# Kernel tuning notes

Hardware: AMD Instinct MI355X
Metric: run time of the kernel (lower is better)

## Reference

```python
import jax, jax.numpy as jnp
import numpy as np
import math

B, S, D = 4, 4096, 1024
H = 16
HD = D // H          # head_dim = 64
M = 256              # nb_features (random projection dim)


def _orthogonal_gaussian(key, m, d):
    # FAVOR+ orthogonal random features: blocks of d orthogonal rows,
    # each row rescaled to a chi-distributed norm (norm of a d-dim gaussian).
    n_blocks = int(math.ceil(m / d))
    keys = jax.random.split(key, n_blocks + 1)
    blocks = []
    for i in range(n_blocks):
        g = jax.random.normal(keys[i], (d, d), dtype=jnp.float32)
        q, _ = jnp.linalg.qr(g)
        blocks.append(q.T)
    W = jnp.concatenate(blocks, axis=0)[:m]  # [m, d]
    norms = jnp.linalg.norm(
        jax.random.normal(keys[-1], (m, d), dtype=jnp.float32), axis=1, keepdims=True)
    return W * norms


def _softmax_kernel(x, proj, is_query, eps=1e-4):
    # x: [b,h,s,d]; proj: [m,d]. Standard FAVOR+ positive softmax features.
    d = x.shape[-1]
    ratio = proj.shape[0] ** -0.5
    x = x * (d ** -0.25)
    u = jnp.einsum('bhsd,md->bhsm', x, proj)  # projection
    diag = 0.5 * jnp.sum(x * x, axis=-1, keepdims=True)  # [b,h,s,1]
    if is_query:
        stab = jnp.max(u, axis=-1, keepdims=True)
    else:
        stab = jnp.max(u, axis=(-1, -2), keepdims=True)
    return ratio * (jnp.exp(u - diag - stab) + eps)


def performer_attention(Q, K, V, mask, proj):
    # Q,K,V: [b,h,s,d], mask: [b,s]
    scale = HD ** -0.25
    m4 = mask[:, None, :, None]
    Qs = Q * scale
    Ks = K * scale * m4
    Vs = V * m4
    q_prime = _softmax_kernel(Qs, proj, is_query=True)   # [b,h,s,m]
    k_prime = _softmax_kernel(Ks, proj, is_query=False)  # [b,h,s,m]
    # linear attention: O(s*m*d)
    kv = jnp.einsum('bhsm,bhsd->bhmd', k_prime, Vs)      # [b,h,m,d]
    z = 1.0 / (jnp.einsum('bhsm,bhm->bhs', q_prime, jnp.sum(k_prime, axis=2)) + 1e-6)
    out = jnp.einsum('bhsm,bhmd->bhsd', q_prime, kv) * z[..., None]
    return out


def setup_inputs() -> dict:
    key = jax.random.key(0)
    ks = jax.random.split(key, 9)
    X = jax.random.normal(ks[0], (B, S, D), dtype=jnp.float32)
    mask = jnp.ones((B, S), dtype=jnp.float32)
    s = D ** -0.5
    Wq = jax.random.normal(ks[1], (D, D), dtype=jnp.float32) * s
    bq = jnp.zeros((D,), dtype=jnp.float32)
    Wk = jax.random.normal(ks[2], (D, D), dtype=jnp.float32) * s
    bk = jnp.zeros((D,), dtype=jnp.float32)
    Wv = jax.random.normal(ks[3], (D, D), dtype=jnp.float32) * s
    bv = jnp.zeros((D,), dtype=jnp.float32)
    proj = _orthogonal_gaussian(ks[4], M, HD)
    return {"X": X, "mask": mask, "Wq": Wq, "bq": bq, "Wk": Wk, "bk": bk,
            "Wv": Wv, "bv": bv, "proj": proj}


def _split_heads(x):
    b, s, _ = x.shape
    return x.reshape(b, s, H, HD).transpose(0, 2, 1, 3)


def reference(X, mask, Wq, bq, Wk, bk, Wv, bv, proj):
    Q = _split_heads(X @ Wq + bq)
    K = _split_heads(X @ Wk + bk)
    V = _split_heads(X @ Wv + bv)
    attn = performer_attention(Q, K, V, mask, proj)  # [b,h,s,hd]
    out = attn.transpose(0, 2, 1, 3).reshape(B, S, D)
    return out
```

## Files before the change

kernel.cpp:

```cpp
#include <hip/hip_runtime.h>
#include <stdint.h>

#define DEVI static __device__ __forceinline__

typedef unsigned short u16;
typedef unsigned int u32;
typedef __attribute__((ext_vector_type(8))) short short8;
typedef __attribute__((ext_vector_type(4))) float f32x4;
typedef __attribute__((ext_vector_type(4))) unsigned short ushort4_t;

#define BB 4
#define SS 4096
#define DD 1024
#define HH 16
#define HDD 64
#define MM 256
#define BHN 64

DEVI u16 f2bf(float f) {
    u32 u = __float_as_uint(f);
    u += 0x7fffu + ((u >> 16) & 1u);
    return (u16)(u >> 16);
}
DEVI float bf2f(u16 h) { return __uint_as_float(((u32)h) << 16); }
DEVI u32 fenc(float f) {
    u32 u = __float_as_uint(f);
    return (u & 0x80000000u) ? ~u : (u | 0x80000000u);
}
DEVI float fdec(u32 k) {
    u32 u = (k & 0x80000000u) ? (k & 0x7fffffffu) : ~k;
    return __uint_as_float(u);
}

typedef __attribute__((address_space(1))) const unsigned int as1_u32;
typedef __attribute__((address_space(3))) unsigned int as3_u32;
DEVI void load_lds16(const void* g, void* lds) {
    __builtin_amdgcn_global_load_lds((as1_u32*)g, (as3_u32*)lds, 16, 0, 0);
}


__global__ void conv_bf16(const float* __restrict__ src, u16* __restrict__ dst, int n4) {
    int i = blockIdx.x * 256 + threadIdx.x;
    if (i < n4) {
        float4 v = reinterpret_cast<const float4*>(src)[i];
        ushort4_t o = { f2bf(v.x), f2bf(v.y), f2bf(v.z), f2bf(v.w) };
        reinterpret_cast<ushort4_t*>(dst)[i] = o;
    }
}

__global__ void conv_w(const float* __restrict__ Wq, const float* __restrict__ Wk,
                       const float* __restrict__ Wv, u16* __restrict__ Wt) {
    __shared__ float tile[64][65];
    const int jt = blockIdx.x, kt = blockIdx.y;
    const float* src = (jt < 16) ? Wq : (jt < 32) ? Wk : Wv;
    const int j0 = (jt & 15) * 64, k0 = kt * 64;
    const int t = threadIdx.x;
    for (int i = 0; i < 16; ++i) {
        int lin = t + i * 256;
        int kl = lin >> 6, jl = lin & 63;
        tile[kl][jl] = src[(size_t)(k0 + kl) * DD + j0 + jl];
    }
    __syncthreads();
    const int jg0 = jt * 64;
    for (int i = 0; i < 16; ++i) {
        int lin = t + i * 256;
        int jl = lin >> 6, kl = lin & 63;
        Wt[(size_t)(jg0 + jl) * DD + k0 + kl] = f2bf(tile[kl][jl]);
    }
}

__global__ __launch_bounds__(512, 2) void gemm1_big(
    const u16* __restrict__ Xbf, const u16* __restrict__ Wt,
    const float* __restrict__ bq, const float* __restrict__ bk, const float* __restrict__ bv,
    const float* __restrict__ mask,
    u16* __restrict__ Qh, u16* __restrict__ Kh, u16* __restrict__ Vt,
    float* __restrict__ dq, float* __restrict__ dk)
{
    extern __shared__ __align__(16) char smem[];
    const int tid = threadIdx.x, l = tid & 63, wv = tid >> 6;
    const int wm = wv >> 2, wn = wv & 3;
    const int bid = blockIdx.x;
    const int xcd = bid & 7, i6 = bid >> 3;
    const int bx = xcd * 8 + i6 / 12, by = i6 % 12;
    const int row0 = bx * 256, col0 = by * 256;

    const int srow = tid >> 3;
    const int scol = ((tid & 7) ^ (srow & 7)) * 8;

    #define ABUF(p) ((char*)smem + (p) * 32768)
    #define BBUF(p) ((char*)smem + 65536 + (p) * 32768)
    #define STA(p, kt, r) load_lds16(Xbf + (size_t)(row0 + (r)*64 + srow) * DD + (kt)*64 + scol, \
                                     ABUF(p) + (r)*8192 + wv*1024)
    #define STB(p, kt, r) load_lds16(Wt + (size_t)(col0 + (r)*64 + srow) * DD + (kt)*64 + scol, \
                                     BBUF(p) + (r)*8192 + wv*1024)

    STA(0,0,0); STA(0,0,1); STA(0,0,2); STA(0,0,3);
    STB(0,0,0); STB(0,0,1); STB(0,0,2); STB(0,0,3);
    asm volatile("s_waitcnt vmcnt(0)" ::: "memory");
    __builtin_amdgcn_s_barrier();
    __builtin_amdgcn_sched_barrier(0);

    f32x4 acc[8][4] = {};
    const int arow_b = wm * 128 + (l & 15);
    const int brow_b = wn * 64 + (l & 15);
    const int cb_b = (l >> 4) * 16;
    const int lx = (l & 7) << 4;

    for (int kt = 0; kt < 16; ++kt) {
        const int p = kt & 1, pn = p ^ 1;
        const bool more = (kt + 1) < 16;
        short8 bfr[4][2];
#pragma unroll
        for (int q = 0; q < 4; ++q) {
            if (more) {
                if (q == 0)      { STA(pn, kt + 1, 0); STA(pn, kt + 1, 1); }
                else if (q == 1) { STA(pn, kt + 1, 2); STA(pn, kt + 1, 3); }
                else if (q == 2) { STB(pn, kt + 1, 0); STB(pn, kt + 1, 1); }
                else             { STB(pn, kt + 1, 2); STB(pn, kt + 1, 3); }
            }
            if (q == 0) {
#pragma unroll
                for (int nf = 0; nf < 4; ++nf) {
                    const int br = brow_b + nf * 16;
#pragma unroll
                    for (int ks = 0; ks < 2; ++ks)
                        bfr[nf][ks] = *(const short8*)(BBUF(p) + br * 128 + ((cb_b + ks * 64) ^ lx));
                }
            }
            short8 a[2][2];
#pragma unroll
            for (int i = 0; i < 2; ++i) {
                const int ar = arow_b + (q * 2 + i) * 16;
#pragma unroll
                for (int ks = 0; ks < 2; ++ks)
                    a[i][ks] = *(const short8*)(ABUF(p) + ar * 128 + ((cb_b + ks * 64) ^ lx));
            }
            __builtin_amdgcn_s_setprio(1);
#pragma unroll
            for (int i = 0; i < 2; ++i)
#pragma unroll
                for (int nf = 0; nf < 4; ++nf) {
                    acc[q*2+i][nf] = __builtin_amdgcn_mfma_f32_16x16x32_bf16(a[i][0], bfr[nf][0], acc[q*2+i][nf], 0, 0, 0);
                    acc[q*2+i][nf] = __builtin_amdgcn_mfma_f32_16x16x32_bf16(a[i][1], bfr[nf][1], acc[q*2+i][nf], 0, 0, 0);
                }
            __builtin_amdgcn_s_setprio(0);
            __builtin_amdgcn_sched_barrier(0);
        }
        asm volatile("s_waitcnt vmcnt(0)" ::: "memory");
        __builtin_amdgcn_s_barrier();
        __builtin_amdgcn_sched_barrier(0);
    }

    const int region = by >> 2;
    const int h = ((by & 3) << 2) + wn;
    const int rg = row0 + wm * 128;
    const int b = rg >> 12;
    const int sb = rg & 4095;
    const size_t bh = (size_t)(b * HH + h);
    const int dd = l & 15;
    const int jbase = ((by & 3) << 8) + wn * 64;

    if (region == 0) {
        float bias[4];
#pragma unroll
        for (int nf = 0; nf < 4; ++nf) bias[nf] = bq[jbase + nf * 16 + dd];
#pragma unroll
        for (int mf = 0; mf < 8; ++mf) {
            float ds4[4];
#pragma unroll
            for (int g = 0; g < 4; ++g) {
                const int s = sb + mf * 16 + ((l >> 4) << 2) + g;
                float dsum = 0.f;
#pragma unroll
                for (int nf = 0; nf < 4; ++nf) {
                    u16 hv = f2bf((acc[mf][nf][g] + bias[nf]) * 0.125f);
                    Qh[(bh * SS + s) * HDD + nf * 16 + dd] = hv;
                    float fv = bf2f(hv);
                    dsum += fv * fv;
                }
                dsum += __shfl_xor(dsum, 1);
                dsum += __shfl_xor(dsum, 2);
                dsum += __shfl_xor(dsum, 4);
                dsum += __shfl_xor(dsum, 8);
                ds4[g] = 0.5f * dsum;
            }
            if (dd == 0)
                *(float4*)(dq + bh * SS + sb + mf * 16 + ((l >> 4) << 2)) =
                    make_float4(ds4[0], ds4[1], ds4[2], ds4[3]);
        }
    } else if (region == 1) {
        float bias[4];
#pragma unroll
        for (int nf = 0; nf < 4; ++nf) bias[nf] = bk[jbase + nf * 16 + dd];
#pragma unroll
        for (int mf = 0; mf < 8; ++mf) {
            float ds4[4];
#pragma unroll
            for (int g = 0; g < 4; ++g) {
                const int s = sb + mf * 16 + ((l >> 4) << 2) + g;
                const float m = mask[b * SS + s];
                float dsum = 0.f;
#pragma unroll
                for (int nf = 0; nf < 4; ++nf) {
                    u16 hv = f2bf((acc[mf][nf][g] + bias[nf]) * m * 0.125f);
                    Kh[(bh * SS + s) * HDD + nf * 16 + dd] = hv;
                    float fv = bf2f(hv);
                    dsum += fv * fv;
                }
                dsum += __shfl_xor(dsum, 1);
                dsum += __shfl_xor(dsum, 2);
                dsum += __shfl_xor(dsum, 4);
                dsum += __shfl_xor(dsum, 8);
                ds4[g] = 0.5f * dsum;
            }
            if (dd == 0)
                *(float4*)(dk + bh * SS + sb + mf * 16 + ((l >> 4) << 2)) =
                    make_float4(ds4[0], ds4[1], ds4[2], ds4[3]);
        }
    } else {
        float bias[4];
#pragma unroll
        for (int nf = 0; nf < 4; ++nf) bias[nf] = bv[jbase + nf * 16 + dd];
#pragma unroll
        for (int mf = 0; mf < 8; ++mf) {
            const int s0 = sb + mf * 16 + ((l >> 4) << 2);
#pragma unroll
            for (int nf = 0; nf < 4; ++nf) {
                ushort4_t pk;
#pragma unroll
                for (int g = 0; g < 4; ++g) {
                    const float m = mask[b * SS + s0 + g];
                    pk[g] = f2bf((acc[mf][nf][g] + bias[nf]) * m);
                }
                *(ushort4_t*)(Vt + (bh * HDD + nf * 16 + dd) * SS + s0) = pk;
            }
        }
    }
    #undef ABUF
    #undef BBUF
    #undef STA
    #undef STB
}

__global__ __launch_bounds__(256, 2) void stab_kernel(
    const u16* __restrict__ Kh, const u16* __restrict__ projb, u32* __restrict__ stabkey)
{
    __shared__ __align__(16) u16 Klds[64 * 64];
    __shared__ float red4[4];
    const int tid = threadIdx.x, l = tid & 63, wv = tid >> 6;
    const int rt = blockIdx.x, bh = blockIdx.y;
    short8 pb[4][2];
#pragma unroll
    for (int nf = 0; nf < 4; ++nf)
#pragma unroll
        for (int ks = 0; ks < 2; ++ks)
            pb[nf][ks] = *(const short8*)(projb + (wv * 64 + nf * 16 + (l & 15)) * HDD + ks * 32 + (l >> 4) * 8);
    const size_t sbase = (size_t)bh * SS + rt * 64;
#pragma unroll
    for (int c = 0; c < 2; ++c) {
        const int rb = wv * 16 + c * 8;
        const int r = rb + (l >> 3);
        load_lds16(Kh + (sbase + r) * HDD + (((l & 7) ^ (r & 7)) * 8), (char*)Klds + rb * 128);
    }
    __syncthreads();
    float mx = -3.0e38f;
#pragma unroll
    for (int sf = 0; sf < 4; ++sf) {
        const int s = sf * 16 + (l & 15);
        f32x4 u4[4] = {};
#pragma unroll
        for (int ks = 0; ks < 2; ++ks) {
            short8 ak = *(const short8*)((const char*)Klds + s * 128 + ((ks * 64 + (l >> 4) * 16) ^ ((s & 7) << 4)));
#pragma unroll
            for (int nf = 0; nf < 4; ++nf)
                u4[nf] = __builtin_amdgcn_mfma_f32_16x16x32_bf16(ak, pb[nf][ks], u4[nf], 0, 0, 0);
        }
#pragma unroll
        for (int nf = 0; nf < 4; ++nf)
#pragma unroll
            for (int g = 0; g < 4; ++g) mx = fmaxf(mx, u4[nf][g]);
    }
#pragma unroll
    for (int o = 1; o < 64; o <<= 1) mx = fmaxf(mx, __shfl_xor(mx, o));
    if (l == 0) red4[wv] = mx;
    __syncthreads();
    if (tid == 0) {
        float m2 = fmaxf(fmaxf(red4[0], red4[1]), fmaxf(red4[2], red4[3]));
        atomicMax(stabkey + bh, fenc(m2));
    }
}

__global__ __launch_bounds__(256, 2) void kv_fused(
    const u16* __restrict__ Kh, const u16* __restrict__ Vt,
    const u16* __restrict__ projb, const float* __restrict__ dk,
    const u32* __restrict__ stabkey,
    float* __restrict__ kv_part, float* __restrict__ ksum_part)
{
    __shared__ __align__(16) u16 Klds[64 * 64];
    __shared__ __align__(16) u16 Vlds[64 * 64];
    __shared__ __align__(16) u16 Kp[256 * 64];
    const int tid = threadIdx.x, l = tid & 63, wv = tid >> 6;
    const int ck = blockIdx.x, bh = blockIdx.y;
    const float stab = fdec(stabkey[bh]);
    short8 pb[4][2];
#pragma unroll
    for (int nf = 0; nf < 4; ++nf)
#pragma unroll
        for (int ks = 0; ks < 2; ++ks)
            pb[nf][ks] = *(const short8*)(projb + (wv * 64 + nf * 16 + (l & 15)) * HDD + ks * 32 + (l >> 4) * 8);
    f32x4 acc[4][4] = {};
    float ksc[4] = {0.f, 0.f, 0.f, 0.f};
    const size_t sbase = (size_t)bh * SS + ck * 512;
    for (int it = 0; it < 8; ++it) {
        const int s0 = it * 64;
#pragma unroll
        for (int c = 0; c < 2; ++c) {
            const int rb = wv * 16 + c * 8;
            const int r = rb + (l >> 3);
            const int sc = ((l & 7) ^ (r & 7)) * 8;
            load_lds16(Kh + (sbase + s0 + r) * HDD + sc, (char*)Klds + rb * 128);
            load_lds16(Vt + ((size_t)bh * HDD + r) * SS + ck * 512 + s0 + sc, (char*)Vlds + rb * 128);
        }
        __syncthreads();
#pragma unroll
        for (int sf = 0; sf < 4; ++sf) {
            const int s = sf * 16 + (l & 15);
            f32x4 u4[4] = {};
#pragma unroll
            for (int ks = 0; ks < 2; ++ks) {
                short8 ak = *(const short8*)((const char*)Klds + s * 128 + ((ks * 64 + (l >> 4) * 16) ^ ((s & 7) << 4)));
#pragma unroll
                for (int nf = 0; nf < 4; ++nf)
                    u4[nf] = __builtin_amdgcn_mfma_f32_16x16x32_bf16(ak, pb[nf][ks], u4[nf], 0, 0, 0);
            }
            const int srow = sf * 16 + (l >> 4) * 4;
            const float4 dkv = *(const float4*)(dk + sbase + s0 + srow);
#pragma unroll
            for (int nf = 0; nf < 4; ++nf) {
                const int m = wv * 64 + nf * 16 + (l & 15);
                u16 h0 = f2bf(0.0625f * (__expf(u4[nf][0] - dkv.x - stab) + 1e-4f));
                u16 h1 = f2bf(0.0625f * (__expf(u4[nf][1] - dkv.y - stab) + 1e-4f));
                u16 h2 = f2bf(0.0625f * (__expf(u4[nf][2] - dkv.z - stab) + 1e-4f));
                u16 h3 = f2bf(0.0625f * (__expf(u4[nf][3] - dkv.w - stab) + 1e-4f));
                ksc[nf] += bf2f(h0) + bf2f(h1) + bf2f(h2) + bf2f(h3);
                uint2 w; w.x = (u32)h0 | ((u32)h1 << 16); w.y = (u32)h2 | ((u32)h3 << 16);
                *(uint2*)((char*)Kp + m * 128 + ((srow * 2) ^ ((m & 7) << 4))) = w;
            }
        }
#pragma unroll
        for (int ks = 0; ks < 2; ++ks) {
            short8 am[4], bv8[4];
#pragma unroll
            for (int mf = 0; mf < 4; ++mf) {
                const int m = wv * 64 + mf * 16 + (l & 15);
                am[mf] = *(const short8*)((const char*)Kp + m * 128 + ((ks * 64 + (l >> 4) * 16) ^ ((m & 7) << 4)));
            }
#pragma unroll
            for (int nf = 0; nf < 4; ++nf) {
                const int d = nf * 16 + (l & 15);
                bv8[nf] = *(const short8*)((const char*)Vlds + d * 128 + ((ks * 64 + (l >> 4) * 16) ^ ((d & 7) << 4)));
            }
#pragma unroll
            for (int mf = 0; mf < 4; ++mf)
#pragma unroll
                for (int nf = 0; nf < 4; ++nf)
                    acc[mf][nf] = __builtin_amdgcn_mfma_f32_16x16x32_bf16(am[mf], bv8[nf], acc[mf][nf], 0, 0, 0);
        }
        __syncthreads();
    }
    const size_t pbase = (size_t)ck * BHN + bh;
#pragma unroll
    for (int nf = 0; nf < 4; ++nf) {
        float v = ksc[nf];
        v += __shfl_xor(v, 16);
        v += __shfl_xor(v, 32);
        if (l < 16) ksum_part[pbase * MM + wv * 64 + nf * 16 + l] = v;
    }
#pragma unroll
    for (int mf = 0; mf < 4; ++mf)
#pragma unroll
        for (int nf = 0; nf < 4; ++nf)
            *(f32x4*)(kv_part + (pbase * HDD + nf * 16 + (l & 15)) * MM + wv * 64 + mf * 16 + (l >> 4) * 4) = acc[mf][nf];
}

__global__ void reduceB2(const float* __restrict__ kv_part, const float* __restrict__ ksum_part,
                         u16* __restrict__ Bmat) {
    const int bh = blockIdx.x, n = blockIdx.y, t = threadIdx.x;
    float s = 0.f;
    if (n < 64) {
#pragma unroll
        for (int ck = 0; ck < 8; ++ck) s += kv_part[(((size_t)ck * BHN + bh) * HDD + n) * MM + t];
    } else if (n == 64) {
#pragma unroll
        for (int ck = 0; ck < 8; ++ck) s += ksum_part[((size_t)ck * BHN + bh) * MM + t];
    }
    Bmat[((size_t)bh * 80 + n) * MM + t] = (n <= 64) ? f2bf(s) : (u16)0;
}

__global__ __launch_bounds__(256, 2) void out_fused(
    const u16* __restrict__ Qh, const u16* __restrict__ projb,
    const float* __restrict__ dq, const u16* __restrict__ Bmat,
    float* __restrict__ out)
{
    __shared__ __align__(16) u16 Blds[80 * 256];
    __shared__ __align__(16) u16 Qlds[32 * 64];
    __shared__ __align__(16) u16 qlds[32 * 256];
    __shared__ float red[4][32];
    const int tid = threadIdx.x, l = tid & 63, wv = tid >> 6;
    const int rt = blockIdx.x, bh = blockIdx.y;
#pragma unroll
    for (int c = 0; c < 10; ++c) {
        const int r = (wv * 10 + c) * 2 + (l >> 5);
        load_lds16(Bmat + (size_t)bh * 20480 + r * 256 + (((l & 31) ^ (r & 7)) * 8),
                   (char*)Blds + (wv * 10 + c) * 1024);
    }
    const size_t srowbase = (size_t)bh * SS + rt * 32;
    {
        const int rb = wv * 8;
        const int r = rb + (l >> 3);
        load_lds16(Qh + (srowbase + r) * HDD + (((l & 7) ^ (r & 7)) * 8), (char*)Qlds + rb * 128);
    }
    short8 pa[4][2];
#pragma unroll
    for (int mf = 0; mf < 4; ++mf)
#pragma unroll
        for (int ks = 0; ks < 2; ++ks)
            pa[mf][ks] = *(const short8*)(projb + (wv * 64 + mf * 16 + (l & 15)) * HDD + ks * 32 + (l >> 4) * 8);
    __syncthreads();
    f32x4 u[4][2] = {};
#pragma unroll
    for (int ks = 0; ks < 2; ++ks) {
        short8 bq8[2];
#pragma unroll
        for (int nf = 0; nf < 2; ++nf) {
            const int s = nf * 16 + (l & 15);
            bq8[nf] = *(const short8*)((const char*)Qlds + s * 128 + ((ks * 64 + (l >> 4) * 16) ^ ((s & 7) << 4)));
        }
#pragma unroll
        for (int mf = 0; mf < 4; ++mf)
#pragma unroll
            for (int nf = 0; nf < 2; ++nf)
                u[mf][nf] = __builtin_amdgcn_mfma_f32_16x16x32_bf16(pa[mf][ks], bq8[nf], u[mf][nf], 0, 0, 0);
    }
#pragma unroll
    for (int nf = 0; nf < 2; ++nf) {
        float v = -3.0e38f;
#pragma unroll
        for (int mf = 0; mf < 4; ++mf)
#pragma unroll
            for (int g = 0; g < 4; ++g) v = fmaxf(v, u[mf][nf][g]);
        v = fmaxf(v, __shfl_xor(v, 16));
        v = fmaxf(v, __shfl_xor(v, 32));
        if ((l >> 4) == 0) red[wv][nf * 16 + l] = v;
    }
    __syncthreads();
#pragma unroll
    for (int nf = 0; nf < 2; ++nf) {
        const int s = nf * 16 + (l & 15);
        const float mx = fmaxf(fmaxf(red[0][s], red[1][s]), fmaxf(red[2][s], red[3][s]));
        const float dg = dq[srowbase + s];
#pragma unroll
        for (int mf = 0; mf < 4; ++mf) {
            u16 h0 = f2bf(0.0625f * (__expf(u[mf][nf][0] - dg - mx) + 1e-4f));
            u16 h1 = f2bf(0.0625f * (__expf(u[mf][nf][1] - dg - mx) + 1e-4f));
            u16 h2 = f2bf(0.0625f * (__expf(u[mf][nf][2] - dg - mx) + 1e-4f));
            u16 h3 = f2bf(0.0625f * (__expf(u[mf][nf][3] - dg - mx) + 1e-4f));
            uint2 w; w.x = (u32)h0 | ((u32)h1 << 16); w.y = (u32)h2 | ((u32)h3 << 16);
            const int mb = (wv * 64 + mf * 16 + (l >> 4) * 4) * 2;
            *(uint2*)((char*)qlds + s * 512 + (mb ^ ((s & 7) << 4))) = w;
        }
    }
    __syncthreads();
    f32x4 acc[2][2] = {};
    for (int kt = 0; kt < 8; ++kt) {
        short8 aq[2], bb[2];
#pragma unroll
        for (int mf = 0; mf < 2; ++mf) {
            const int s = mf * 16 + (l & 15);
            aq[mf] = *(const short8*)((const char*)qlds + s * 512 + ((kt * 64 + (l >> 4) * 16) ^ ((s & 7) << 4)));
        }
        {
            const int n0 = wv * 16 + (l & 15);
            bb[0] = *(const short8*)((const char*)Blds + n0 * 512 + ((kt * 64 + (l >> 4) * 16) ^ ((n0 & 7) << 4)));
            const int n1 = 64 + (l & 15);
            bb[1] = *(const short8*)((const char*)Blds + n1 * 512 + ((kt * 64 + (l >> 4) * 16) ^ ((n1 & 7) << 4)));
        }
#pragma unroll
        for (int mf = 0; mf < 2; ++mf)
#pragma unroll
            for (int nf = 0; nf < 2; ++nf)
                acc[mf][nf] = __builtin_amdgcn_mfma_f32_16x16x32_bf16(aq[mf], bb[nf], acc[mf][nf], 0, 0, 0);
    }
    const int b = bh >> 4, h = bh & 15;
#pragma unroll
    for (int mf = 0; mf < 2; ++mf) {
#pragma unroll
        for (int g = 0; g < 4; ++g) {
            const float den = __shfl(acc[mf][1][g], (l & 48));
            const float z = 1.0f / (den + 1e-6f);
            const int s = rt * 32 + mf * 16 + (l >> 4) * 4 + g;
            out[((size_t)b * SS + s) * DD + h * HDD + wv * 16 + (l & 15)] = acc[mf][0][g] * z;
        }
    }
}

extern "C" void kernel_launch(void* const* d_in, const int* in_sizes, int n_in,
                              void* d_out, int out_size, void* d_ws, size_t ws_size,
                              hipStream_t stream)
{
    const float* X    = (const float*)d_in[0];
    const float* mask = (const float*)d_in[1];
    const float* Wq   = (const float*)d_in[2];
    const float* bq   = (const float*)d_in[3];
    const float* Wk   = (const float*)d_in[4];
    const float* bk   = (const float*)d_in[5];
    const float* Wv   = (const float*)d_in[6];
    const float* bv   = (const float*)d_in[7];
    const float* proj = (const float*)d_in[8];
    float* out = (float*)d_out;

    char* p = (char*)d_ws;
    u16* Xbf = (u16*)p;
    float* kv_part = (float*)p; p += 33554432;
    u16* Wt = (u16*)p;    p += 6291456;
    u16* projb = (u16*)p; p += 32768;
    u16* Qh = (u16*)p;    p += 33554432;
    u16* Kh = (u16*)p;    p += 33554432;
    u16* Vt = (u16*)p;    p += 33554432;
    float* dq = (float*)p; p += 1048576;
    float* dk = (float*)p; p += 1048576;
    u32* stabkey = (u32*)p; p += 256;
    float* ksum_part = (float*)p; p += 524288;
    u16* Bmat = (u16*)p;  p += 2621440;
    if (ws_size < 145785088ull) return;

    hipFuncSetAttribute((const void*)gemm1_big, hipFuncAttributeMaxDynamicSharedMemorySize, 131072);

    hipMemsetAsync(stabkey, 0, 256, stream);
    conv_bf16<<<16384, 256, 0, stream>>>(X, Xbf, 4194304);
    conv_w<<<dim3(48, 16), 256, 0, stream>>>(Wq, Wk, Wv, Wt);
    conv_bf16<<<16, 256, 0, stream>>>(proj, projb, 4096);
    gemm1_big<<<768, 512, 131072, stream>>>(Xbf, Wt, bq, bk, bv, mask, Qh, Kh, Vt, dq, dk);
    stab_kernel<<<dim3(64, 64), 256, 0, stream>>>(Kh, projb, stabkey);
    kv_fused<<<dim3(8, 64), 256, 0, stream>>>(Kh, Vt, projb, dk, stabkey, kv_part, ksum_part);
    reduceB2<<<dim3(64, 80), 256, 0, stream>>>(kv_part, ksum_part, Bmat);
    out_fused<<<dim3(128, 64), 256, 0, stream>>>(Qh, projb, dq, Bmat, out);
}
```

Before: 298.4 us.

## Use K=32 tiles with 4-stage LDS pipeline in QKV projection GEMM

The QKV projection GEMM's K step shrinks from 64 to 32. The LDS ring grows from double to quadruple buffering, so loads are issued three iterations ahead and waits use partial vmcnt counts instead of draining to zero. The LDS layout is remapped so that two 32-wide rows pack into each 128-byte line with an XOR swizzle, giving one short8 read per fragment. The aim is to hide global load latency better, at the cost of twice as many barriers and a more intricate address mapping.

Measured after the change: 305.1 us. 2.2% more time.

```diff
diff --git a/kernel.cpp b/kernel.cpp
--- a/kernel.cpp
+++ b/kernel.cpp
@@ -69,7 +69,7 @@
     }
 }
 
-__global__ __launch_bounds__(512, 2) void gemm1_big(
+__global__ __launch_bounds__(512, 2) void gemm1_k32(
     const u16* __restrict__ Xbf, const u16* __restrict__ Wt,
     const float* __restrict__ bq, const float* __restrict__ bk, const float* __restrict__ bv,
     const float* __restrict__ mask,
@@ -84,71 +84,72 @@
     const int bx = xcd * 8 + i6 / 12, by = i6 % 12;
     const int row0 = bx * 256, col0 = by * 256;
 
-    const int srow = tid >> 3;
-    const int scol = ((tid & 7) ^ (srow & 7)) * 8;
-
-    #define ABUF(p) ((char*)smem + (p) * 32768)
-    #define BBUF(p) ((char*)smem + 65536 + (p) * 32768)
-    #define STA(p, kt, r) load_lds16(Xbf + (size_t)(row0 + (r)*64 + srow) * DD + (kt)*64 + scol, \
-                                     ABUF(p) + (r)*8192 + wv*1024)
-    #define STB(p, kt, r) load_lds16(Wt + (size_t)(col0 + (r)*64 + srow) * DD + (kt)*64 + scol, \
-                                     BBUF(p) + (r)*8192 + wv*1024)
-
-    STA(0,0,0); STA(0,0,1); STA(0,0,2); STA(0,0,3);
-    STB(0,0,0); STB(0,0,1); STB(0,0,2); STB(0,0,3);
-    asm volatile("s_waitcnt vmcnt(0)" ::: "memory");
+    int sA[2];
+#pragma unroll
+    for (int j = 0; j < 2; ++j) {
+        const int o = j * 8192 + tid * 16;
+        const int R = o >> 7;
+        const int logpos = (o & 127) ^ ((R & 7) << 4);
+        const int r = 2 * R + (logpos >> 6);
+        const int c8 = (logpos >> 4) & 3;
+        sA[j] = r * DD + c8 * 8;
+    }
+    const size_t xbase = (size_t)row0 * DD;
+    const size_t wbase = (size_t)col0 * DD;
+
+    #define ABUF(b) ((char*)smem + (b) * 16384)
+    #define BBUF(b) ((char*)smem + 65536 + (b) * 16384)
+    #define STA(b, kt, j) load_lds16(Xbf + xbase + (kt) * 32 + sA[j], ABUF(b) + (j) * 8192 + wv * 1024)
+    #define STB(b, kt, j) load_lds16(Wt + wbase + (kt) * 32 + sA[j], BBUF(b) + (j) * 8192 + wv * 1024)
+
+#pragma unroll
+    for (int t = 0; t < 3; ++t) { STA(t, t, 0); STA(t, t, 1); STB(t, t, 0); STB(t, t, 1); }
+    asm volatile("s_waitcnt vmcnt(8)" ::: "memory");
     __builtin_amdgcn_s_barrier();
     __builtin_amdgcn_sched_barrier(0);
 
     f32x4 acc[8][4] = {};
-    const int arow_b = wm * 128 + (l & 15);
-    const int brow_b = wn * 64 + (l & 15);
-    const int cb_b = (l >> 4) * 16;
-    const int lx = (l & 7) << 4;
-
-    for (int kt = 0; kt < 16; ++kt) {
-        const int p = kt & 1, pn = p ^ 1;
-        const bool more = (kt + 1) < 16;
-        short8 bfr[4][2];
+    const int hl = (l & 15) >> 1;
+    const int xorc = hl << 4;
+    const int pa = ((wm * 64 + hl) * 128 + (l & 1) * 64 + (l >> 4) * 16) ^ xorc;
+    const int pb = ((wn * 32 + hl) * 128 + (l & 1) * 64 + (l >> 4) * 16) ^ xorc;
+
+    for (int kt = 0; kt < 32; ++kt) {
+        const int p = kt & 3, pn = (kt + 3) & 3;
+        const bool more = (kt + 3) < 32;
+        short8 bfr[4];
 #pragma unroll
         for (int q = 0; q < 4; ++q) {
             if (more) {
-                if (q == 0)      { STA(pn, kt + 1, 0); STA(pn, kt + 1, 1); }
-                else if (q == 1) { STA(pn, kt + 1, 2); STA(pn, kt + 1, 3); }
-                else if (q == 2) { STB(pn, kt + 1, 0); STB(pn, kt + 1, 1); }
-                else             { STB(pn, kt + 1, 2); STB(pn, kt + 1, 3); }
+                if (q == 0)      STA(pn, kt + 3, 0);
+                else if (q == 1) STA(pn, kt + 3, 1);
+                else if (q == 2) STB(pn, kt + 3, 0);
+                else             STB(pn, kt + 3, 1);
             }
             if (q == 0) {
 #pragma unroll
-                for (int nf = 0; nf < 4; ++nf) {
-                    const int br = brow_b + nf * 16;
-#pragma unroll
-                    for (int ks = 0; ks < 2; ++ks)
-                        bfr[nf][ks] = *(const short8*)(BBUF(p) + br * 128 + ((cb_b + ks * 64) ^ lx));
-                }
-            }
-            short8 a[2][2];
-#pragma unroll
-            for (int i = 0; i < 2; ++i) {
-                const int ar = arow_b + (q * 2 + i) * 16;
-#pragma unroll
-                for (int ks = 0; ks < 2; ++ks)
-                    a[i][ks] = *(const short8*)(ABUF(p) + ar * 128 + ((cb_b + ks * 64) ^ lx));
-            }
+                for (int nf = 0; nf < 4; ++nf)
+                    bfr[nf] = *(const short8*)(BBUF(p) + pb + nf * 1024);
+            }
+            short8 a[2];
+#pragma unroll
+            for (int i = 0; i < 2; ++i)
+                a[i] = *(const short8*)(ABUF(p) + pa + (q * 2 + i) * 1024);
             __builtin_amdgcn_s_setprio(1);
 #pragma unroll
             for (int i = 0; i < 2; ++i)
 #pragma unroll
-                for (int nf = 0; nf < 4; ++nf) {
-                    acc[q*2+i][nf] = __builtin_amdgcn_mfma_f32_16x16x32_bf16(a[i][0], bfr[nf][0], acc[q*2+i][nf], 0, 0, 0);
-                    acc[q*2+i][nf] = __builtin_amdgcn_mfma_f32_16x16x32_bf16(a[i][1], bfr[nf][1], acc[q*2+i][nf], 0, 0, 0);
-                }
+                for (int nf = 0; nf < 4; ++nf)
+                    acc[q * 2 + i][nf] = __builtin_amdgcn_mfma_f32_16x16x32_bf16(a[i], bfr[nf], acc[q * 2 + i][nf], 0, 0, 0);
             __builtin_amdgcn_s_setprio(0);
+        }
+        if (kt < 31) {
+            if (kt + 3 < 32)      asm volatile("s_waitcnt vmcnt(8)" ::: "memory");
+            else if (kt + 2 < 32) asm volatile("s_waitcnt vmcnt(4)" ::: "memory");
+            else                  asm volatile("s_waitcnt vmcnt(0)" ::: "memory");
+            __builtin_amdgcn_s_barrier();
             __builtin_amdgcn_sched_barrier(0);
         }
-        asm volatile("s_waitcnt vmcnt(0)" ::: "memory");
-        __builtin_amdgcn_s_barrier();
-        __builtin_amdgcn_sched_barrier(0);
     }
 
     const int region = by >> 2;
@@ -534,13 +535,13 @@
     u16* Bmat = (u16*)p;  p += 2621440;
     if (ws_size < 145785088ull) return;
 
-    hipFuncSetAttribute((const void*)gemm1_big, hipFuncAttributeMaxDynamicSharedMemorySize, 131072);
+    hipFuncSetAttribute((const void*)gemm1_k32, hipFuncAttributeMaxDynamicSharedMemorySize, 131072);
 
     hipMemsetAsync(stabkey, 0, 256, stream);
     conv_bf16<<<16384, 256, 0, stream>>>(X, Xbf, 4194304);
     conv_w<<<dim3(48, 16), 256, 0, stream>>>(Wq, Wk, Wv, Wt);
     conv_bf16<<<16, 256, 0, stream>>>(proj, projb, 4096);
-    gemm1_big<<<768, 512, 131072, stream>>>(Xbf, Wt, bq, bk, bv, mask, Qh, Kh, Vt, dq, dk);
+    gemm1_k32<<<768, 512, 131072, stream>>>(Xbf, Wt, bq, bk, bv, mask, Qh, Kh, Vt, dq, dk);
     stab_kernel<<<dim3(64, 64), 256, 0, stream>>>(Kh, projb, stabkey);
     kv_fused<<<dim3(8, 64), 256, 0, stream>>>(Kh, Vt, projb, dk, stabkey, kv_part, ksum_part);
     reduceB2<<<dim3(64, 80), 256, 0, stream>>>(kv_part, ksum_part, Bmat);
```

## Fold key stabilizer into kv pass with per-chunk local max and rescale in reduce

Applied to the files above, without the earlier changes.

Drops the separate stab_kernel, its atomicMax and the memset. Each kv_fused block now computes a per-wave local max over its 512-row chunk, using triple-buffered async K loads, and then builds kv and ksum against that local stabilizer. The epsilon term is moved out via a separately accumulated V sum. reduceB3 rescales each chunk's partials by exp(local-global) and adds the eps and ratio terms. out_fused now processes 64 rows per block and reads Bmat straight from global memory instead of staging it in LDS. The cost is a second pass over K per chunk inside kv_fused and a change in numerics from per-chunk stabilization.

New measurement: 260.1 us. -12.8%, faster.

```diff
diff --git a/kernel.cpp b/kernel.cpp
--- a/kernel.cpp
+++ b/kernel.cpp
@@ -23,14 +23,6 @@
     return (u16)(u >> 16);
 }
 DEVI float bf2f(u16 h) { return __uint_as_float(((u32)h) << 16); }
-DEVI u32 fenc(float f) {
-    u32 u = __float_as_uint(f);
-    return (u & 0x80000000u) ? ~u : (u | 0x80000000u);
-}
-DEVI float fdec(u32 k) {
-    u32 u = (k & 0x80000000u) ? (k & 0x7fffffffu) : ~k;
-    return __uint_as_float(u);
-}
 
 typedef __attribute__((address_space(1))) const unsigned int as1_u32;
 typedef __attribute__((address_space(3))) unsigned int as3_u32;
@@ -242,111 +234,121 @@
     #undef STB
 }
 
-__global__ __launch_bounds__(256, 2) void stab_kernel(
-    const u16* __restrict__ Kh, const u16* __restrict__ projb, u32* __restrict__ stabkey)
-{
-    __shared__ __align__(16) u16 Klds[64 * 64];
-    __shared__ float red4[4];
-    const int tid = threadIdx.x, l = tid & 63, wv = tid >> 6;
-    const int rt = blockIdx.x, bh = blockIdx.y;
-    short8 pb[4][2];
-#pragma unroll
-    for (int nf = 0; nf < 4; ++nf)
-#pragma unroll
-        for (int ks = 0; ks < 2; ++ks)
-            pb[nf][ks] = *(const short8*)(projb + (wv * 64 + nf * 16 + (l & 15)) * HDD + ks * 32 + (l >> 4) * 8);
-    const size_t sbase = (size_t)bh * SS + rt * 64;
-#pragma unroll
-    for (int c = 0; c < 2; ++c) {
-        const int rb = wv * 16 + c * 8;
-        const int r = rb + (l >> 3);
-        load_lds16(Kh + (sbase + r) * HDD + (((l & 7) ^ (r & 7)) * 8), (char*)Klds + rb * 128);
-    }
-    __syncthreads();
-    float mx = -3.0e38f;
-#pragma unroll
-    for (int sf = 0; sf < 4; ++sf) {
-        const int s = sf * 16 + (l & 15);
-        f32x4 u4[4] = {};
-#pragma unroll
-        for (int ks = 0; ks < 2; ++ks) {
-            short8 ak = *(const short8*)((const char*)Klds + s * 128 + ((ks * 64 + (l >> 4) * 16) ^ ((s & 7) << 4)));
-#pragma unroll
-            for (int nf = 0; nf < 4; ++nf)
-                u4[nf] = __builtin_amdgcn_mfma_f32_16x16x32_bf16(ak, pb[nf][ks], u4[nf], 0, 0, 0);
-        }
-#pragma unroll
-        for (int nf = 0; nf < 4; ++nf)
-#pragma unroll
-            for (int g = 0; g < 4; ++g) mx = fmaxf(mx, u4[nf][g]);
-    }
-#pragma unroll
-    for (int o = 1; o < 64; o <<= 1) mx = fmaxf(mx, __shfl_xor(mx, o));
-    if (l == 0) red4[wv] = mx;
-    __syncthreads();
-    if (tid == 0) {
-        float m2 = fmaxf(fmaxf(red4[0], red4[1]), fmaxf(red4[2], red4[3]));
-        atomicMax(stabkey + bh, fenc(m2));
-    }
-}
-
 __global__ __launch_bounds__(256, 2) void kv_fused(
     const u16* __restrict__ Kh, const u16* __restrict__ Vt,
     const u16* __restrict__ projb, const float* __restrict__ dk,
-    const u32* __restrict__ stabkey,
-    float* __restrict__ kv_part, float* __restrict__ ksum_part)
+    float* __restrict__ kv_part, float* __restrict__ ksum_part,
+    float* __restrict__ vsum_part, float* __restrict__ lstab)
 {
-    __shared__ __align__(16) u16 Klds[64 * 64];
-    __shared__ __align__(16) u16 Vlds[64 * 64];
-    __shared__ __align__(16) u16 Kp[256 * 64];
+    extern __shared__ __align__(16) char ksm[];
+    #define KLDS(b) ((char*)ksm + (b) * 8192)
+    #define VLDS(b) ((char*)ksm + 24576 + (b) * 8192)
+    u16* Kp = (u16*)((char*)ksm + 49152);
     const int tid = threadIdx.x, l = tid & 63, wv = tid >> 6;
     const int ck = blockIdx.x, bh = blockIdx.y;
-    const float stab = fdec(stabkey[bh]);
     short8 pb[4][2];
 #pragma unroll
     for (int nf = 0; nf < 4; ++nf)
 #pragma unroll
         for (int ks = 0; ks < 2; ++ks)
             pb[nf][ks] = *(const short8*)(projb + (wv * 64 + nf * 16 + (l & 15)) * HDD + ks * 32 + (l >> 4) * 8);
-    f32x4 acc[4][4] = {};
-    float ksc[4] = {0.f, 0.f, 0.f, 0.f};
     const size_t sbase = (size_t)bh * SS + ck * 512;
+
+    #define KSTAGE(buf, it8) do { \
+        const int s0_ = (it8) * 64; \
+        _Pragma("unroll") \
+        for (int c = 0; c < 2; ++c) { \
+            const int rb = wv * 16 + c * 8; \
+            const int r = rb + (l >> 3); \
+            const int sc = ((l & 7) ^ (r & 7)) * 8; \
+            load_lds16(Kh + (sbase + s0_ + r) * HDD + sc, KLDS(buf) + rb * 128); \
+        } \
+    } while (0)
+    #define VSTAGE(buf, it8) do { \
+        const int s0_ = (it8) * 64; \
+        _Pragma("unroll") \
+        for (int c = 0; c < 2; ++c) { \
+            const int rb = wv * 16 + c * 8; \
+            const int r = rb + (l >> 3); \
+            const int sc = ((l & 7) ^ (r & 7)) * 8; \
+            load_lds16(Vt + ((size_t)bh * HDD + r) * SS + ck * 512 + s0_ + sc, VLDS(buf) + rb * 128); \
+        } \
+    } while (0)
+
+    float wmax = -3.0e38f;
+    KSTAGE(0, 0);
     for (int it = 0; it < 8; ++it) {
-        const int s0 = it * 64;
-#pragma unroll
-        for (int c = 0; c < 2; ++c) {
-            const int rb = wv * 16 + c * 8;
-            const int r = rb + (l >> 3);
-            const int sc = ((l & 7) ^ (r & 7)) * 8;
-            load_lds16(Kh + (sbase + s0 + r) * HDD + sc, (char*)Klds + rb * 128);
-            load_lds16(Vt + ((size_t)bh * HDD + r) * SS + ck * 512 + s0 + sc, (char*)Vlds + rb * 128);
+        if (it + 1 < 8) {
+            KSTAGE((it + 1) % 3, it + 1);
+            asm volatile("s_waitcnt vmcnt(2)" ::: "memory");
+        } else {
+            asm volatile("s_waitcnt vmcnt(0)" ::: "memory");
         }
         __syncthreads();
+        const int bs = it % 3;
 #pragma unroll
         for (int sf = 0; sf < 4; ++sf) {
             const int s = sf * 16 + (l & 15);
             f32x4 u4[4] = {};
 #pragma unroll
             for (int ks = 0; ks < 2; ++ks) {
-                short8 ak = *(const short8*)((const char*)Klds + s * 128 + ((ks * 64 + (l >> 4) * 16) ^ ((s & 7) << 4)));
+                short8 ak = *(const short8*)(KLDS(bs) + s * 128 + ((ks * 64 + (l >> 4) * 16) ^ ((s & 7) << 4)));
 #pragma unroll
                 for (int nf = 0; nf < 4; ++nf)
                     u4[nf] = __builtin_amdgcn_mfma_f32_16x16x32_bf16(ak, pb[nf][ks], u4[nf], 0, 0, 0);
             }
+#pragma unroll
+            for (int nf = 0; nf < 4; ++nf)
+#pragma unroll
+                for (int g = 0; g < 4; ++g) wmax = fmaxf(wmax, u4[nf][g]);
+        }
+    }
+#pragma unroll
+    for (int o = 1; o < 64; o <<= 1) wmax = fmaxf(wmax, __shfl_xor(wmax, o));
+    if (l == 0) lstab[((size_t)ck * BHN + bh) * 4 + wv] = wmax;
+    const float stab = wmax;
+
+    f32x4 acc[4][4] = {};
+    float ksc[4] = {0.f, 0.f, 0.f, 0.f};
+    float vsc[4] = {0.f, 0.f, 0.f, 0.f};
+    KSTAGE(0, 0); VSTAGE(0, 0);
+    for (int it = 0; it < 8; ++it) {
+        if (it + 1 < 8) {
+            KSTAGE((it + 1) % 3, it + 1);
+            VSTAGE((it + 1) % 3, it + 1);
+            asm volatile("s_waitcnt vmcnt(4)" ::: "memory");
+        } else {
+            asm volatile("s_waitcnt vmcnt(0)" ::: "memory");
+        }
+        __syncthreads();
+        const int bs = it % 3;
+        const int s0 = it * 64;
+#pragma unroll
+        for (int sf = 0; sf < 4; ++sf) {
+            const int s = sf * 16 + (l & 15);
+            f32x4 u4[4] = {};
+#pragma unroll
+            for (int ks = 0; ks < 2; ++ks) {
+                short8 ak = *(const short8*)(KLDS(bs) + s * 128 + ((ks * 64 + (l >> 4) * 16) ^ ((s & 7) << 4)));
+#pragma unroll
+                for (int nf = 0; nf < 4; ++nf)
+                    u4[nf] = __builtin_amdgcn_mfma_f32_16x16x32_bf16(ak, pb[nf][ks], u4[nf], 0, 0, 0);
+            }
             const int srow = sf * 16 + (l >> 4) * 4;
             const float4 dkv = *(const float4*)(dk + sbase + s0 + srow);
 #pragma unroll
             for (int nf = 0; nf < 4; ++nf) {
                 const int m = wv * 64 + nf * 16 + (l & 15);
-                u16 h0 = f2bf(0.0625f * (__expf(u4[nf][0] - dkv.x - stab) + 1e-4f));
-                u16 h1 = f2bf(0.0625f * (__expf(u4[nf][1] - dkv.y - stab) + 1e-4f));
-                u16 h2 = f2bf(0.0625f * (__expf(u4[nf][2] - dkv.z - stab) + 1e-4f));
-                u16 h3 = f2bf(0.0625f * (__expf(u4[nf][3] - dkv.w - stab) + 1e-4f));
+                u16 h0 = f2bf(__expf(u4[nf][0] - dkv.x - stab));
+                u16 h1 = f2bf(__expf(u4[nf][1] - dkv.y - stab));
+                u16 h2 = f2bf(__expf(u4[nf][2] - dkv.z - stab));
+                u16 h3 = f2bf(__expf(u4[nf][3] - dkv.w - stab));
                 ksc[nf] += bf2f(h0) + bf2f(h1) + bf2f(h2) + bf2f(h3);
                 uint2 w; w.x = (u32)h0 | ((u32)h1 << 16); w.y = (u32)h2 | ((u32)h3 << 16);
                 *(uint2*)((char*)Kp + m * 128 + ((srow * 2) ^ ((m & 7) << 4))) = w;
             }
         }
+        __syncthreads();
 #pragma unroll
         for (int ks = 0; ks < 2; ++ks) {
             short8 am[4], bv8[4];
@@ -358,7 +360,11 @@
 #pragma unroll
             for (int nf = 0; nf < 4; ++nf) {
                 const int d = nf * 16 + (l & 15);
-                bv8[nf] = *(const short8*)((const char*)Vlds + d * 128 + ((ks * 64 + (l >> 4) * 16) ^ ((d & 7) << 4)));
+                bv8[nf] = *(const short8*)(VLDS(bs) + d * 128 + ((ks * 64 + (l >> 4) * 16) ^ ((d & 7) << 4)));
+                float vs = 0.f;
+#pragma unroll
+                for (int e = 0; e < 8; ++e) vs += bf2f((u16)bv8[nf][e]);
+                vsc[nf] += vs;
             }
 #pragma unroll
             for (int mf = 0; mf < 4; ++mf)
@@ -366,7 +372,6 @@
                 for (int nf = 0; nf < 4; ++nf)
                     acc[mf][nf] = __builtin_amdgcn_mfma_f32_16x16x32_bf16(am[mf], bv8[nf], acc[mf][nf], 0, 0, 0);
         }
-        __syncthreads();
     }
     const size_t pbase = (size_t)ck * BHN + bh;
 #pragma unroll
@@ -375,48 +380,68 @@
         v += __shfl_xor(v, 16);
         v += __shfl_xor(v, 32);
         if (l < 16) ksum_part[pbase * MM + wv * 64 + nf * 16 + l] = v;
+        float w = vsc[nf];
+        w += __shfl_xor(w, 16);
+        w += __shfl_xor(w, 32);
+        if (wv == 0 && l < 16) vsum_part[pbase * HDD + nf * 16 + l] = w;
     }
 #pragma unroll
     for (int mf = 0; mf < 4; ++mf)
 #pragma unroll
         for (int nf = 0; nf < 4; ++nf)
             *(f32x4*)(kv_part + (pbase * HDD + nf * 16 + (l & 15)) * MM + wv * 64 + mf * 16 + (l >> 4) * 4) = acc[mf][nf];
-}
-
-__global__ void reduceB2(const float* __restrict__ kv_part, const float* __restrict__ ksum_part,
+    #undef KLDS
+    #undef VLDS
+    #undef KSTAGE
+    #undef VSTAGE
+}
+
+__global__ void reduceB3(const float* __restrict__ kv_part, const float* __restrict__ ksum_part,
+                         const float* __restrict__ vsum_part, const float* __restrict__ lstab,
                          u16* __restrict__ Bmat) {
+    __shared__ float f[8][4];
     const int bh = blockIdx.x, n = blockIdx.y, t = threadIdx.x;
+    if (t < 32) {
+        float lv = lstab[((size_t)(t >> 2) * BHN + bh) * 4 + (t & 3)];
+        float g = lv;
+#pragma unroll
+        for (int o = 1; o < 32; o <<= 1) g = fmaxf(g, __shfl_xor(g, o));
+        f[t >> 2][t & 3] = __expf(lv - g);
+    }
+    __syncthreads();
+    const int grp = t >> 6;
     float s = 0.f;
     if (n < 64) {
-#pragma unroll
-        for (int ck = 0; ck < 8; ++ck) s += kv_part[(((size_t)ck * BHN + bh) * HDD + n) * MM + t];
+        float vsg = 0.f;
+#pragma unroll
+        for (int ck = 0; ck < 8; ++ck) {
+            vsg += vsum_part[((size_t)ck * BHN + bh) * HDD + n];
+            s += kv_part[(((size_t)ck * BHN + bh) * HDD + n) * MM + t] * f[ck][grp];
+        }
+        s = 0.0625f * (s + 1e-4f * vsg);
     } else if (n == 64) {
 #pragma unroll
-        for (int ck = 0; ck < 8; ++ck) s += ksum_part[((size_t)ck * BHN + bh) * MM + t];
+        for (int ck = 0; ck < 8; ++ck)
+            s += ksum_part[((size_t)ck * BHN + bh) * MM + t] * f[ck][grp];
+        s = 0.0625f * (s + 1e-4f * 4096.0f);
     }
     Bmat[((size_t)bh * 80 + n) * MM + t] = (n <= 64) ? f2bf(s) : (u16)0;
 }
 
-__global__ __launch_bounds__(256, 2) void out_fused(
+__global__ __launch_bounds__(256) void out_fused(
     const u16* __restrict__ Qh, const u16* __restrict__ projb,
     const float* __restrict__ dq, const u16* __restrict__ Bmat,
     float* __restrict__ out)
 {
-    __shared__ __align__(16) u16 Blds[80 * 256];
-    __shared__ __align__(16) u16 Qlds[32 * 64];
-    __shared__ __align__(16) u16 qlds[32 * 256];
-    __shared__ float red[4][32];
+    __shared__ __align__(16) u16 Qlds[64 * 64];
+    __shared__ __align__(16) u16 qlds[64 * 256];
+    __shared__ float red[4][64];
     const int tid = threadIdx.x, l = tid & 63, wv = tid >> 6;
     const int rt = blockIdx.x, bh = blockIdx.y;
-#pragma unroll
-    for (int c = 0; c < 10; ++c) {
-        const int r = (wv * 10 + c) * 2 + (l >> 5);
-        load_lds16(Bmat + (size_t)bh * 20480 + r * 256 + (((l & 31) ^ (r & 7)) * 8),
-                   (char*)Blds + (wv * 10 + c) * 1024);
-    }
-    const size_t srowbase = (size_t)bh * SS + rt * 32;
-    {
-        const int rb = wv * 8;
+    const size_t srowbase = (size_t)bh * SS + rt * 64;
+#pragma unroll
+    for (int c = 0; c < 2; ++c) {
+        const int rb = wv * 16 + c * 8;
         const int r = rb + (l >> 3);
         load_lds16(Qh + (srowbase + r) * HDD + (((l & 7) ^ (r & 7)) * 8), (char*)Qlds + rb * 128);
     }
@@ -427,23 +452,23 @@
         for (int ks = 0; ks < 2; ++ks)
             pa[mf][ks] = *(const short8*)(projb + (wv * 64 + mf * 16 + (l & 15)) * HDD + ks * 32 + (l >> 4) * 8);
     __syncthreads();
-    f32x4 u[4][2] = {};
+    f32x4 u[4][4] = {};
 #pragma unroll
     for (int ks = 0; ks < 2; ++ks) {
-        short8 bq8[2];
-#pragma unroll
-        for (int nf = 0; nf < 2; ++nf) {
+        short8 bq8[4];
+#pragma unroll
+        for (int nf = 0; nf < 4; ++nf) {
             const int s = nf * 16 + (l & 15);
             bq8[nf] = *(const short8*)((const char*)Qlds + s * 128 + ((ks * 64 + (l >> 4) * 16) ^ ((s & 7) << 4)));
         }
 #pragma unroll
         for (int mf = 0; mf < 4; ++mf)
 #pragma unroll
-            for (int nf = 0; nf < 2; ++nf)
+            for (int nf = 0; nf < 4; ++nf)
                 u[mf][nf] = __builtin_amdgcn_mfma_f32_16x16x32_bf16(pa[mf][ks], bq8[nf], u[mf][nf], 0, 0, 0);
     }
 #pragma unroll
-    for (int nf = 0; nf < 2; ++nf) {
+    for (int nf = 0; nf < 4; ++nf) {
         float v = -3.0e38f;
 #pragma unroll
         for (int mf = 0; mf < 4; ++mf)
@@ -455,7 +480,7 @@
     }
     __syncthreads();
 #pragma unroll
-    for (int nf = 0; nf < 2; ++nf) {
+    for (int nf = 0; nf < 4; ++nf) {
         const int s = nf * 16 + (l & 15);
         const float mx = fmaxf(fmaxf(red[0][s], red[1][s]), fmaxf(red[2][s], red[3][s]));
         const float dg = dq[srowbase + s];
@@ -471,34 +496,32 @@
         }
     }
     __syncthreads();
-    f32x4 acc[2][2] = {};
+    const u16* bbase = Bmat + (size_t)bh * 20480;
+    f32x4 acc[4][2] = {};
+#pragma unroll
     for (int kt = 0; kt < 8; ++kt) {
-        short8 aq[2], bb[2];
-#pragma unroll
-        for (int mf = 0; mf < 2; ++mf) {
+        short8 aq[4], bb[2];
+#pragma unroll
+        for (int mf = 0; mf < 4; ++mf) {
             const int s = mf * 16 + (l & 15);
             aq[mf] = *(const short8*)((const char*)qlds + s * 512 + ((kt * 64 + (l >> 4) * 16) ^ ((s & 7) << 4)));
         }
-        {
-            const int n0 = wv * 16 + (l & 15);
-            bb[0] = *(const short8*)((const char*)Blds + n0 * 512 + ((kt * 64 + (l >> 4) * 16) ^ ((n0 & 7) << 4)));
-            const int n1 = 64 + (l & 15);
-            bb[1] = *(const short8*)((const char*)Blds + n1 * 512 + ((kt * 64 + (l >> 4) * 16) ^ ((n1 & 7) << 4)));
-        }
-#pragma unroll
-        for (int mf = 0; mf < 2; ++mf)
+        bb[0] = *(const short8*)(bbase + (wv * 16 + (l & 15)) * 256 + kt * 32 + (l >> 4) * 8);
+        bb[1] = *(const short8*)(bbase + (64 + (l & 15)) * 256 + kt * 32 + (l >> 4) * 8);
+#pragma unroll
+        for (int mf = 0; mf < 4; ++mf)
 #pragma unroll
             for (int nf = 0; nf < 2; ++nf)
                 acc[mf][nf] = __builtin_amdgcn_mfma_f32_16x16x32_bf16(aq[mf], bb[nf], acc[mf][nf], 0, 0, 0);
     }
     const int b = bh >> 4, h = bh & 15;
 #pragma unroll
-    for (int mf = 0; mf < 2; ++mf) {
+    for (int mf = 0; mf < 4; ++mf) {
 #pragma unroll
         for (int g = 0; g < 4; ++g) {
             const float den = __shfl(acc[mf][1][g], (l & 48));
             const float z = 1.0f / (den + 1e-6f);
-            const int s = rt * 32 + mf * 16 + (l >> 4) * 4 + g;
+            const int s = rt * 64 + mf * 16 + (l >> 4) * 4 + g;
             out[((size_t)b * SS + s) * DD + h * HDD + wv * 16 + (l & 15)] = acc[mf][0][g] * z;
         }
     }
@@ -529,20 +552,20 @@
     u16* Vt = (u16*)p;    p += 33554432;
     float* dq = (float*)p; p += 1048576;
     float* dk = (float*)p; p += 1048576;
-    u32* stabkey = (u32*)p; p += 256;
     float* ksum_part = (float*)p; p += 524288;
     u16* Bmat = (u16*)p;  p += 2621440;
-    if (ws_size < 145785088ull) return;
+    float* vsum_part = (float*)p; p += 131072;
+    float* lstab = (float*)p; p += 8192;
+    if (ws_size < 145924096ull) return;
 
     hipFuncSetAttribute((const void*)gemm1_big, hipFuncAttributeMaxDynamicSharedMemorySize, 131072);
-
-    hipMemsetAsync(stabkey, 0, 256, stream);
+    hipFuncSetAttribute((const void*)kv_fused, hipFuncAttributeMaxDynamicSharedMemorySize, 81920);
+
     conv_bf16<<<16384, 256, 0, stream>>>(X, Xbf, 4194304);
     conv_w<<<dim3(48, 16), 256, 0, stream>>>(Wq, Wk, Wv, Wt);
     conv_bf16<<<16, 256, 0, stream>>>(proj, projb, 4096);
     gemm1_big<<<768, 512, 131072, stream>>>(Xbf, Wt, bq, bk, bv, mask, Qh, Kh, Vt, dq, dk);
-    stab_kernel<<<dim3(64, 64), 256, 0, stream>>>(Kh, projb, stabkey);
-    kv_fused<<<dim3(8, 64), 256, 0, stream>>>(Kh, Vt, projb, dk, stabkey, kv_part, ksum_part);
-    reduceB2<<<dim3(64, 80), 256, 0, stream>>>(kv_part, ksum_part, Bmat);
-    out_fused<<<dim3(128, 64), 256, 0, stream>>>(Qh, projb, dq, Bmat, out);
-}
+    kv_fused<<<dim3(8, 64), 256, 81920, stream>>>(Kh, Vt, projb, dk, kv_part, ksum_part, vsum_part, lstab);
+    reduceB3<<<dim3(64, 80), 256, 0, stream>>>(kv_part, ksum_part, vsum_part, lstab, Bmat);
+    out_fused<<<dim3(64, 64), 256, 0, stream>>>(Qh, projb, dq, Bmat, out);
+}
```
